# Kernel tuning notes

Hardware: AMD Instinct MI355X
Metric: run time of the kernel (lower is better)

Reference implementation:

```python
import jax, jax.numpy as jnp
import numpy as np

IMAGE_W = 256
IMAGE_H = 256
SIGMA = 0.2
EPS = 1e-07


def _gauss_filter(g, size, psize, pad):
    """g: [B,N] center coords in pixels. Returns [B,N,size,psize]."""
    # grid coords over padded canvas: value i - pad at row i (matches np.indices - pad)
    coords = jnp.arange(size + 2 * pad, dtype=jnp.float32) - pad          # [size+2pad]
    offs = jnp.arange(1, psize + 1, dtype=jnp.float32) - psize / 2 - 0.5  # [psize]
    mu = g[:, :, None] + offs[None, None, :]                              # [B,N,psize]
    F = jnp.exp(-(coords[None, None, :, None] - mu[:, :, None, :]) ** 2 / (2 * SIGMA ** 2))
    F = F / (F.sum(axis=2, keepdims=True) + EPS)
    return F[:, :, pad:size + pad]                                        # [B,N,size,psize]


def setup_inputs() -> dict:
    key = jax.random.key(0)
    k1, k2 = jax.random.split(key)
    brushes = jax.random.uniform(k1, (32, 64, 2), dtype=jnp.float32)
    patches = jax.random.normal(k2, (32, 64, 3, 16, 16), dtype=jnp.float32)
    return {"brushes": brushes, "patches": patches}


def reference(brushes, patches):
    B, N, C, ph, pw = patches.shape
    pad = ph // 2  # pad='half_patch'
    gx = brushes[:, :, 0] * IMAGE_W  # [B,N]
    gy = brushes[:, :, 1] * IMAGE_H
    Fx = _gauss_filter(gx, IMAGE_W, pw, pad)  # [B,N,w,pw]
    Fy = _gauss_filter(gy, IMAGE_H, ph, pad)  # [B,N,h,ph]
    # contract over pw: [B,N,C,w,ph]
    t = jnp.einsum('bnwq,bncpq->bncwp', Fx, patches)
    # contract over ph: [B,N,C,w,h]
    out = jnp.einsum('bncwp,bnhp->bncwh', t, Fy)
    out = out.mean(axis=1)            # [B,C,w,h]
    out = jnp.swapaxes(out, 2, 3)     # [B,C,h,w]
    return out
```

## Files before the change

kernel.cpp:

```cpp
#include <hip/hip_runtime.h>


__global__ __launch_bounds__(256) void zero_out(float4* __restrict__ out)
{
    out[blockIdx.x * 256 + threadIdx.x] = make_float4(0.f, 0.f, 0.f, 0.f);
}

__global__ __launch_bounds__(256) void brush_scatter(
        const float* __restrict__ brushes,
        const float* __restrict__ patches,
        float* __restrict__ out)
{
    const int n   = blockIdx.x;
    const int b   = blockIdx.y;
    const int tid = threadIdx.x;

    __shared__ float P[3 * 256];
    __shared__ float wT[2][22][5];
    __shared__ int   qloT[2][22];
    __shared__ float T[3 * 352];

    const int bn = (b << 6) + n;
    const float gx = brushes[2 * bn]     * 256.0f;
    const float gy = brushes[2 * bn + 1] * 256.0f;
    const int x0 = (int)floorf(gx) - 10;
    const int y0 = (int)floorf(gy) - 10;

    const float* pb = patches + (size_t)bn * 768;
    P[tid]       = pb[tid];
    P[tid + 256] = pb[tid + 256];
    P[tid + 512] = pb[tid + 512];

    if (tid < 220) {
        const int axis = tid / 110;
        const int r    = tid - axis * 110;
        const int i    = r / 5;
        const int j    = r - i * 5;
        const float g    = axis ? gy : gx;
        const float wpos = (float)((axis ? y0 : x0) + i);
        const float a    = wpos - g + 7.5f;
        int qlo = (int)ceilf(a - 2.5f);
        qlo = qlo < 0 ? 0 : (qlo > 11 ? 11 : qlo);
        const int q = qlo + j;
        const float mu = g + (float)q - 7.5f;
        const float fl = floorf(mu);
        float Z = 0.0f;
#pragma unroll
        for (int d = -1; d <= 2; ++d) {
            const float c = fl + (float)d;
            if (c >= -8.0f && c <= 263.0f) {
                const float u = c - mu;
                Z += __expf(-12.5f * u * u);
            }
        }
        const float dd  = wpos - mu;
        float wgt = __expf(-12.5f * dd * dd) / (Z + 1e-7f);
        if (axis == 0) wgt *= 0.015625f;
        wT[axis][i][j] = wgt;
        if (j == 0) qloT[axis][i] = qlo;
    }
    __syncthreads();

    for (int it = tid; it < 352; it += 256) {
        const int p = it / 22;
        const int i = it - p * 22;
        const int qlo = qloT[0][i];
        const float w0 = wT[0][i][0], w1 = wT[0][i][1], w2 = wT[0][i][2],
                    w3 = wT[0][i][3], w4 = wT[0][i][4];
        const float* Pp = &P[p * 16 + qlo];
#pragma unroll
        for (int c = 0; c < 3; ++c) {
            const float* Pc = Pp + c * 256;
            T[c * 352 + p * 22 + i] =
                w0 * Pc[0] + w1 * Pc[1] + w2 * Pc[2] + w3 * Pc[3] + w4 * Pc[4];
        }
    }
    __syncthreads();

    float* ob = out + ((size_t)(b * 3) << 16);
    for (int e = tid; e < 484; e += 256) {
        const int yi = e / 22;
        const int xi = e - yi * 22;
        const int h = y0 + yi;
        const int w = x0 + xi;
        if (((unsigned)h < 256u) & ((unsigned)w < 256u)) {
            const int plo = qloT[1][yi];
            const float w0 = wT[1][yi][0], w1 = wT[1][yi][1], w2 = wT[1][yi][2],
                        w3 = wT[1][yi][3], w4 = wT[1][yi][4];
            float v0, v1, v2;
            {
                const float* Tc = &T[0 * 352 + plo * 22 + xi];
                v0 = w0*Tc[0] + w1*Tc[22] + w2*Tc[44] + w3*Tc[66] + w4*Tc[88];
            }
            {
                const float* Tc = &T[1 * 352 + plo * 22 + xi];
                v1 = w0*Tc[0] + w1*Tc[22] + w2*Tc[44] + w3*Tc[66] + w4*Tc[88];
            }
            {
                const float* Tc = &T[2 * 352 + plo * 22 + xi];
                v2 = w0*Tc[0] + w1*Tc[22] + w2*Tc[44] + w3*Tc[66] + w4*Tc[88];
            }
            if (fabsf(v0) + fabsf(v1) + fabsf(v2) > 1e-12f) {
                const int off = (h << 8) + w;
                atomicAdd(ob + off,               v0);
                atomicAdd(ob + off + (1 << 16),   v1);
                atomicAdd(ob + off + (2 << 16),   v2);
            }
        }
    }
}

extern "C" void kernel_launch(void* const* d_in, const int* in_sizes, int n_in,
                              void* d_out, int out_size, void* d_ws, size_t ws_size,
                              hipStream_t stream) {
    const float* brushes = (const float*)d_in[0];
    const float* patches = (const float*)d_in[1];
    float* out = (float*)d_out;
    zero_out<<<dim3(6144), dim3(256), 0, stream>>>((float4*)out);
    brush_scatter<<<dim3(64, 32), dim3(256), 0, stream>>>(brushes, patches, out);
}
```

Measured before the change: 81.51 us.

## Replace atomic scatter with per-brush footprint buffer and tile-based gather

The single scatter kernel with its zero-fill pass is split in two. The first kernel writes each brush's 22x22x3 footprint to a workspace buffer. The second kernel assigns each 16x16 output tile to a block, builds a ballot mask of the brushes that overlap that tile, and sums their footprint values with plain stores. This removes the zeroing pass and the global atomic contention. In exchange it adds a workspace round-trip of about 9 MB and a sequential per-tile loop over overlapping brushes.

```diff
diff --git a/kernel.cpp b/kernel.cpp
--- a/kernel.cpp
+++ b/kernel.cpp
@@ -1,15 +1,10 @@
 #include <hip/hip_runtime.h>
 
 
-__global__ __launch_bounds__(256) void zero_out(float4* __restrict__ out)
-{
-    out[blockIdx.x * 256 + threadIdx.x] = make_float4(0.f, 0.f, 0.f, 0.f);
-}
-
-__global__ __launch_bounds__(256) void brush_scatter(
+__global__ __launch_bounds__(256) void brush_prep(
         const float* __restrict__ brushes,
         const float* __restrict__ patches,
-        float* __restrict__ out)
+        float* __restrict__ F)
 {
     const int n   = blockIdx.x;
     const int b   = blockIdx.y;
@@ -77,37 +72,72 @@
     }
     __syncthreads();
 
-    float* ob = out + ((size_t)(b * 3) << 16);
+    float* Fb = F + (size_t)bn * 1452;
     for (int e = tid; e < 484; e += 256) {
         const int yi = e / 22;
         const int xi = e - yi * 22;
-        const int h = y0 + yi;
-        const int w = x0 + xi;
-        if (((unsigned)h < 256u) & ((unsigned)w < 256u)) {
-            const int plo = qloT[1][yi];
-            const float w0 = wT[1][yi][0], w1 = wT[1][yi][1], w2 = wT[1][yi][2],
-                        w3 = wT[1][yi][3], w4 = wT[1][yi][4];
-            float v0, v1, v2;
-            {
-                const float* Tc = &T[0 * 352 + plo * 22 + xi];
-                v0 = w0*Tc[0] + w1*Tc[22] + w2*Tc[44] + w3*Tc[66] + w4*Tc[88];
-            }
-            {
-                const float* Tc = &T[1 * 352 + plo * 22 + xi];
-                v1 = w0*Tc[0] + w1*Tc[22] + w2*Tc[44] + w3*Tc[66] + w4*Tc[88];
-            }
-            {
-                const float* Tc = &T[2 * 352 + plo * 22 + xi];
-                v2 = w0*Tc[0] + w1*Tc[22] + w2*Tc[44] + w3*Tc[66] + w4*Tc[88];
-            }
-            if (fabsf(v0) + fabsf(v1) + fabsf(v2) > 1e-12f) {
-                const int off = (h << 8) + w;
-                atomicAdd(ob + off,               v0);
-                atomicAdd(ob + off + (1 << 16),   v1);
-                atomicAdd(ob + off + (2 << 16),   v2);
-            }
+        const int plo = qloT[1][yi];
+        const float w0 = wT[1][yi][0], w1 = wT[1][yi][1], w2 = wT[1][yi][2],
+                    w3 = wT[1][yi][3], w4 = wT[1][yi][4];
+        const float* T0 = &T[0 * 352 + plo * 22 + xi];
+        const float* T1 = &T[1 * 352 + plo * 22 + xi];
+        const float* T2 = &T[2 * 352 + plo * 22 + xi];
+        Fb[e]       = w0*T0[0] + w1*T0[22] + w2*T0[44] + w3*T0[66] + w4*T0[88];
+        Fb[e + 484] = w0*T1[0] + w1*T1[22] + w2*T1[44] + w3*T1[66] + w4*T1[88];
+        Fb[e + 968] = w0*T2[0] + w1*T2[22] + w2*T2[44] + w3*T2[66] + w4*T2[88];
+    }
+}
+
+__global__ __launch_bounds__(256) void tile_gather(
+        const float* __restrict__ brushes,
+        const float* __restrict__ F,
+        float* __restrict__ out)
+{
+    const int b   = blockIdx.z;
+    const int tx  = blockIdx.x * 16;
+    const int ty  = blockIdx.y * 16;
+    const int tid = threadIdx.x;
+    const int qi  = tid & 15;
+    const int pi  = tid >> 4;
+    const int w   = tx + qi;
+    const int h   = ty + pi;
+
+    __shared__ int2 org[64];
+    __shared__ unsigned long long smask;
+
+    if (tid < 64) {
+        float2 g = ((const float2*)brushes)[(b << 6) + tid];
+        const int x0 = (int)floorf(g.x * 256.0f) - 10;
+        const int y0 = (int)floorf(g.y * 256.0f) - 10;
+        org[tid] = make_int2(x0, y0);
+        const bool hit = (x0 <= tx + 15) & (x0 + 21 >= tx) &
+                         (y0 <= ty + 15) & (y0 + 21 >= ty);
+        const unsigned long long m = __ballot(hit);
+        if (tid == 0) smask = m;
+    }
+    __syncthreads();
+
+    unsigned long long mask = smask;
+    float a0 = 0.0f, a1 = 0.0f, a2 = 0.0f;
+    const size_t bbase = (size_t)(b << 6) * 1452;
+    while (mask) {
+        const int n = __builtin_ctzll(mask);
+        mask &= mask - 1;
+        const int2 o = org[n];
+        const int xi = w - o.x;
+        const int yi = h - o.y;
+        if (((unsigned)xi < 22u) & ((unsigned)yi < 22u)) {
+            const float* f = F + bbase + (size_t)n * 1452 + yi * 22 + xi;
+            a0 += f[0];
+            a1 += f[484];
+            a2 += f[968];
         }
     }
+
+    float* ob = out + (((size_t)(b * 3)) << 16) + (h << 8) + w;
+    ob[0]       = a0;
+    ob[1 << 16] = a1;
+    ob[2 << 16] = a2;
 }
 
 extern "C" void kernel_launch(void* const* d_in, const int* in_sizes, int n_in,
@@ -116,6 +146,7 @@
     const float* brushes = (const float*)d_in[0];
     const float* patches = (const float*)d_in[1];
     float* out = (float*)d_out;
-    zero_out<<<dim3(6144), dim3(256), 0, stream>>>((float4*)out);
-    brush_scatter<<<dim3(64, 32), dim3(256), 0, stream>>>(brushes, patches, out);
+    float* F   = (float*)d_ws;
+    brush_prep<<<dim3(64, 32), dim3(256), 0, stream>>>(brushes, patches, F);
+    tile_gather<<<dim3(16, 16, 32), dim3(256), 0, stream>>>(brushes, F, out);
 }
```

New measurement: 80.05 us. About the same (-1.8%).
